# Kernel tuning notes

Hardware: AMD Instinct MI355X
Metric: run time of the kernel (lower is better)

The kernel has to match this reference:

```python
import jax, jax.numpy as jnp
import numpy as np


def setup_inputs() -> dict:
    key = jax.random.key(0)
    ks = jax.random.split(key, 6)
    B, Q, K = 4, 512, 1024
    Dq, Dk, Dv, H = 512, 512, 512, 128
    return {
        "queries": jax.random.normal(ks[0], (B, Q, Dq), dtype=jnp.float32),
        "keys": jax.random.normal(ks[1], (B, K, Dk), dtype=jnp.float32),
        "values": jax.random.normal(ks[2], (B, K, Dv), dtype=jnp.float32),
        "W_q": jax.random.normal(ks[3], (Dq, H), dtype=jnp.float32) / np.sqrt(Dq),
        "W_k": jax.random.normal(ks[4], (Dk, H), dtype=jnp.float32) / np.sqrt(Dk),
        "w_v": jax.random.normal(ks[5], (H,), dtype=jnp.float32) / np.sqrt(H),
    }


def reference(queries, keys, values, W_q, W_k, w_v):
    # Additive (Bahdanau) attention.
    q = jnp.einsum("bqd,dh->bqh", queries, W_q)          # [B,Q,H]
    k = jnp.einsum("bkd,dh->bkh", keys, W_k)             # [B,K,H]
    features = jnp.tanh(q[:, :, None, :] + k[:, None, :, :])  # [B,Q,K,H]
    scores = jnp.einsum("bqkh,h->bqk", features, w_v)    # [B,Q,K]
    attn = jax.nn.softmax(scores, axis=-1)               # [B,Q,K]
    return jnp.einsum("bqk,bkv->bqv", attn, values)      # [B,Q,Dv]
```

## Files before the change

kernel.cpp:

```cpp
#include <hip/hip_runtime.h>

#define BB   4
#define QS   512
#define KSZ  1024
#define DD   512
#define HH   128
#define DVV  512

typedef unsigned int uint;
typedef unsigned short ushort;
typedef __attribute__((ext_vector_type(8)))  short short8;
typedef __attribute__((ext_vector_type(16))) float f32x16;

__device__ __forceinline__ float rcp_fast(float x)  { return __builtin_amdgcn_rcpf(x); }
__device__ __forceinline__ float exp2_fast(float x) { return __builtin_amdgcn_exp2f(x); }

__device__ __forceinline__ void split1(float v, ushort& h, ushort& l) {
    uint u = __float_as_uint(v);
    h = (ushort)(u >> 16);
    float r = v - __uint_as_float(u & 0xffff0000u);
    l = (ushort)(__float_as_uint(r) >> 16);
}

#define NSQ  (BB * QS * DD / 4 / 256)
#define NSK  (BB * KSZ * DD / 4 / 256)
#define NWT  128
#define NPJ  192
#define NVT  (BB * (KSZ / 32) * (DVV / 32))

__global__ __launch_bounds__(256) void split_kernel(
    const float* __restrict__ q, const float* __restrict__ k,
    const float* __restrict__ Wq, const float* __restrict__ Wk,
    ushort* __restrict__ qh, ushort* __restrict__ ql,
    ushort* __restrict__ kh, ushort* __restrict__ kl,
    ushort* __restrict__ wqh, ushort* __restrict__ wql,
    ushort* __restrict__ wkh, ushort* __restrict__ wkl)
{
    const int id  = blockIdx.x;
    const int tid = threadIdx.x;

    if (id < NSQ + NSK) {
        const float* src; ushort* dh; ushort* dl; size_t i;
        if (id < NSQ) { src = q; dh = qh; dl = ql; i = (size_t)id * 256 + tid; }
        else          { src = k; dh = kh; dl = kl; i = (size_t)(id - NSQ) * 256 + tid; }
        float4 v = ((const float4*)src)[i];
        ushort h0,h1,h2,h3,l0,l1,l2,l3;
        split1(v.x,h0,l0); split1(v.y,h1,l1); split1(v.z,h2,l2); split1(v.w,h3,l3);
        *(ushort4*)&dh[i * 4] = make_ushort4(h0,h1,h2,h3);
        *(ushort4*)&dl[i * 4] = make_ushort4(l0,l1,l2,l3);
        return;
    }
    __shared__ float Ts[32][33];
    int t = id - (NSQ + NSK);
    const float* W; ushort* dh; ushort* dl;
    if (t < 64) { W = Wq; dh = wqh; dl = wql; }
    else        { W = Wk; dh = wkh; dl = wkl; t -= 64; }
    const int d0 = (t >> 2) * 32, h0 = (t & 3) * 32;
    {
        const int dd = tid >> 3, c4 = (tid & 7) * 4;
        float4 v = *(const float4*)&W[(size_t)(d0 + dd) * HH + h0 + c4];
        Ts[dd][c4 + 0] = v.x; Ts[dd][c4 + 1] = v.y;
        Ts[dd][c4 + 2] = v.z; Ts[dd][c4 + 3] = v.w;
    }
    __syncthreads();
    {
        const int hh = tid >> 3, d4 = (tid & 7) * 4;
        ushort h[4], l[4];
        #pragma unroll
        for (int i = 0; i < 4; i++) split1(Ts[d4 + i][hh], h[i], l[i]);
        size_t o = (size_t)(h0 + hh) * DD + d0 + d4;
        *(ushort4*)&dh[o] = make_ushort4(h[0], h[1], h[2], h[3]);
        *(ushort4*)&dl[o] = make_ushort4(l[0], l[1], l[2], l[3]);
    }
}

__global__ __launch_bounds__(256) void projvt_kernel(
    const ushort* __restrict__ qh, const ushort* __restrict__ ql,
    const ushort* __restrict__ kh, const ushort* __restrict__ kl,
    const ushort* __restrict__ wqh, const ushort* __restrict__ wql,
    const ushort* __restrict__ wkh, const ushort* __restrict__ wkl,
    const float* __restrict__ val,
    float* __restrict__ eq, float* __restrict__ ek,
    ushort* __restrict__ vhi, ushort* __restrict__ vlo)
{
    const int id  = blockIdx.x;
    const int tid = threadIdx.x;

    if (id >= NPJ) {
        __shared__ float Ts[32][33];
        const int t   = id - NPJ;
        const int b   = t >> 9;
        const int rem = t & 511;
        const int k0  = (rem >> 4) * 32;
        const int n0  = (rem & 15) * 32;
        {
            const int kk = tid >> 3, n4 = (tid & 7) * 4;
            float4 v = *(const float4*)&val[((size_t)b * KSZ + k0 + kk) * DVV + n0 + n4];
            Ts[kk][n4 + 0] = v.x; Ts[kk][n4 + 1] = v.y;
            Ts[kk][n4 + 2] = v.z; Ts[kk][n4 + 3] = v.w;
        }
        __syncthreads();
        {
            const int nn = tid >> 3, k4 = (tid & 7) * 4;
            ushort h[4], l[4];
            #pragma unroll
            for (int i = 0; i < 4; i++) split1(Ts[k4 + i][nn], h[i], l[i]);
            size_t o = ((size_t)b * DVV + n0 + nn) * KSZ + k0 + k4;
            *(ushort4*)&vhi[o] = make_ushort4(h[0], h[1], h[2], h[3]);
            *(ushort4*)&vlo[o] = make_ushort4(l[0], l[1], l[2], l[3]);
        }
        return;
    }

    const int w = tid >> 6, lane = tid & 63;
    const int row = lane & 31, kg = lane >> 5;
    const int gw = id * 4 + w;

    const ushort *pa_h, *pa_l, *pb_h, *pb_l; float* op; int m0, nt;
    if (gw < 256) {
        m0 = (gw >> 2) * 32; nt = gw & 3;
        pa_h = qh; pa_l = ql; pb_h = wqh; pb_l = wql; op = eq;
    } else {
        const int g = gw - 256;
        m0 = (g >> 2) * 32; nt = g & 3;
        pa_h = kh; pa_l = kl; pb_h = wkh; pb_l = wkl; op = ek;
    }

    const ushort* ah_p = pa_h + (size_t)(m0 + row) * DD + kg * 8;
    const ushort* al_p = pa_l + (size_t)(m0 + row) * DD + kg * 8;
    const ushort* bh_p = pb_h + (size_t)(nt * 32 + row) * DD + kg * 8;
    const ushort* bl_p = pb_l + (size_t)(nt * 32 + row) * DD + kg * 8;

    f32x16 acc;
    #pragma unroll
    for (int i = 0; i < 16; i++) acc[i] = 0.f;

    #pragma unroll 8
    for (int ks = 0; ks < DD; ks += 16) {
        short8 ah = *(const short8*)(ah_p + ks);
        short8 al = *(const short8*)(al_p + ks);
        short8 bh = *(const short8*)(bh_p + ks);
        short8 bl = *(const short8*)(bl_p + ks);
        acc = __builtin_amdgcn_mfma_f32_32x32x16_bf16(ah, bh, acc, 0, 0, 0);
        acc = __builtin_amdgcn_mfma_f32_32x32x16_bf16(ah, bl, acc, 0, 0, 0);
        acc = __builtin_amdgcn_mfma_f32_32x32x16_bf16(al, bh, acc, 0, 0, 0);
    }

    const float C2L = 2.8853900817779268f;
    float* ob = op + (size_t)m0 * HH + nt * 32;
    #pragma unroll
    for (int r = 0; r < 16; r++) {
        const int rb = (r & 3) + 8 * (r >> 2) + 4 * kg;
        ob[(size_t)rb * HH + row] = exp2_fast(acc[r] * C2L);
    }
}

__global__ __launch_bounds__(256) void scores_kernel(
    const float* __restrict__ eq, const float* __restrict__ ek,
    const float* __restrict__ wv, ushort* __restrict__ Phi,
    ushort* __restrict__ Plo, float* __restrict__ rsp)
{
    __shared__ float eqs[64][68];
    __shared__ float eks[64][68];

    const int tid = threadIdx.x;
    const int b  = blockIdx.z;
    const int q0 = blockIdx.y * 64;
    const int k0 = blockIdx.x * 64;

    const float* eqb = eq + ((size_t)b * QS  + q0) * HH;
    const float* ekb = ek + ((size_t)b * KSZ + k0) * HH;

    const int tk = tid & 15;
    const int tq = tid >> 4;

    float acc[4][4] = {};

    for (int hc = 0; hc < HH; hc += 64) {
        __syncthreads();
        #pragma unroll
        for (int i = 0; i < 4; i++) {
            int f = tid + i * 256;
            int row = f >> 4, c4 = f & 15;
            *(float4*)&eqs[row][c4 * 4] =
                *(const float4*)&eqb[(size_t)row * HH + hc + c4 * 4];
            *(float4*)&eks[row][c4 * 4] =
                *(const float4*)&ekb[(size_t)row * HH + hc + c4 * 4];
        }
        __syncthreads();

        for (int h0 = 0; h0 < 64; h0 += 4) {
            float4 wv4 = *(const float4*)&wv[hc + h0];
            float4 eq4[4], ek4[4];
            #pragma unroll
            for (int j = 0; j < 4; j++) {
                eq4[j] = *(const float4*)&eqs[tq + 16 * j][h0];
                ek4[j] = *(const float4*)&eks[tk + 16 * j][h0];
            }
            #pragma unroll
            for (int jq = 0; jq < 4; jq++) {
                #pragma unroll
                for (int jk = 0; jk < 4; jk++) {
                    float u0 = fminf(fmaf(eq4[jq].x, ek4[jk].x, 1.0f), 3e7f);
                    float u1 = fminf(fmaf(eq4[jq].y, ek4[jk].y, 1.0f), 3e7f);
                    float u2 = fminf(fmaf(eq4[jq].z, ek4[jk].z, 1.0f), 3e7f);
                    float u3 = fminf(fmaf(eq4[jq].w, ek4[jk].w, 1.0f), 3e7f);
                    float p01 = u0 * u1, p23 = u2 * u3;
                    float n01 = fmaf(wv4.x, u1, wv4.y * u0);
                    float n23 = fmaf(wv4.z, u3, wv4.w * u2);
                    float N = fmaf(n01, p23, n23 * p01);
                    acc[jq][jk] = fmaf(N, rcp_fast(p01 * p23), acc[jq][jk]);
                }
            }
        }
    }

    const float CN = -2.8853900817779268f;
    ushort* ph = Phi + ((size_t)b * QS + q0) * KSZ + k0;
    ushort* pl = Plo + ((size_t)b * QS + q0) * KSZ + k0;
    #pragma unroll
    for (int jq = 0; jq < 4; jq++) {
        float rowp = 0.f;
        #pragma unroll
        for (int jk = 0; jk < 4; jk++) {
            float pv_ = exp2_fast(acc[jq][jk] * CN);
            ushort hh, ll; split1(pv_, hh, ll);
            size_t o = (size_t)(tq + 16 * jq) * KSZ + tk + 16 * jk;
            ph[o] = hh; pl[o] = ll;
            rowp += pv_;
        }
        #pragma unroll
        for (int m = 8; m; m >>= 1) rowp += __shfl_xor(rowp, m);
        if ((tid & 15) == 0)
            rsp[((size_t)b * QS + q0 + tq + 16 * jq) * 16 + blockIdx.x] = rowp;
    }
}

__global__ __launch_bounds__(256) void pv_mfma_kernel(
    const ushort* __restrict__ Phi, const ushort* __restrict__ Plo,
    const ushort* __restrict__ vhi, const ushort* __restrict__ vlo,
    const float* __restrict__ rsp, float* __restrict__ outp)
{
    __shared__ float invs[32];
    __shared__ float accs[2][32][33];

    const int id  = blockIdx.x;
    const int x   = id & 7;
    const int j   = id >> 3;
    const int bm  = x * 8 + (j >> 3);
    const int ntp = j & 7;
    const int b   = bm >> 4, mt = bm & 15;

    const int tid = threadIdx.x, w = tid >> 6, lane = tid & 63;
    const int row = lane & 31, kg = lane >> 5;

    if (tid < 32) {
        const float* rp = rsp + ((size_t)b * QS + mt * 32 + tid) * 16;
        float s = 0.f;
        #pragma unroll
        for (int i = 0; i < 16; i++) s += rp[i];
        invs[tid] = rcp_fast(s);
    }

    const int nt  = ntp * 2 + (w >> 1);
    const int kh0 = (w & 1) * (KSZ / 2);

    const ushort* pah = Phi + ((size_t)b * QS  + mt * 32 + row) * KSZ + kh0 + kg * 8;
    const ushort* pal = Plo + ((size_t)b * QS  + mt * 32 + row) * KSZ + kh0 + kg * 8;
    const ushort* bhp = vhi + ((size_t)b * DVV + nt * 32 + row) * KSZ + kh0 + kg * 8;
    const ushort* blp = vlo + ((size_t)b * DVV + nt * 32 + row) * KSZ + kh0 + kg * 8;

    f32x16 acc0, acc1;
    #pragma unroll
    for (int i = 0; i < 16; i++) { acc0[i] = 0.f; acc1[i] = 0.f; }

    #pragma unroll 4
    for (int kb = 0; kb < KSZ / 2; kb += 32) {
        short8 a0h = *(const short8*)(pah + kb);
        short8 a0l = *(const short8*)(pal + kb);
        short8 v0h = *(const short8*)(bhp + kb);
        short8 v0l = *(const short8*)(blp + kb);
        short8 a1h = *(const short8*)(pah + kb + 16);
        short8 a1l = *(const short8*)(pal + kb + 16);
        short8 v1h = *(const short8*)(bhp + kb + 16);
        short8 v1l = *(const short8*)(blp + kb + 16);
        acc0 = __builtin_amdgcn_mfma_f32_32x32x16_bf16(a0h, v0h, acc0, 0, 0, 0);
        acc1 = __builtin_amdgcn_mfma_f32_32x32x16_bf16(a1h, v1h, acc1, 0, 0, 0);
        acc0 = __builtin_amdgcn_mfma_f32_32x32x16_bf16(a0h, v0l, acc0, 0, 0, 0);
        acc1 = __builtin_amdgcn_mfma_f32_32x32x16_bf16(a1h, v1l, acc1, 0, 0, 0);
        acc0 = __builtin_amdgcn_mfma_f32_32x32x16_bf16(a0l, v0h, acc0, 0, 0, 0);
        acc1 = __builtin_amdgcn_mfma_f32_32x32x16_bf16(a1l, v1h, acc1, 0, 0, 0);
    }
    #pragma unroll
    for (int i = 0; i < 16; i++) acc0[i] += acc1[i];

    if (w & 1) {
        #pragma unroll
        for (int r = 0; r < 16; r++)
            accs[w >> 1][(r & 3) + 8 * (r >> 2) + 4 * kg][row] = acc0[r];
    }
    __syncthreads();
    if (!(w & 1)) {
        float* ob = outp + ((size_t)b * QS + mt * 32) * DVV + nt * 32;
        #pragma unroll
        for (int r = 0; r < 16; r++) {
            const int rb = (r & 3) + 8 * (r >> 2) + 4 * kg;
            float v = acc0[r] + accs[w >> 1][rb][row];
            ob[(size_t)rb * DVV + row] = v * invs[rb];
        }
    }
}

extern "C" void kernel_launch(void* const* d_in, const int* in_sizes, int n_in,
                              void* d_out, int out_size, void* d_ws, size_t ws_size,
                              hipStream_t stream)
{
    const float* queries = (const float*)d_in[0];
    const float* keys    = (const float*)d_in[1];
    const float* values  = (const float*)d_in[2];
    const float* Wq      = (const float*)d_in[3];
    const float* Wk      = (const float*)d_in[4];
    const float* wv      = (const float*)d_in[5];
    float* out = (float*)d_out;

    float*  eq  = (float*)d_ws;
    float*  ek  = eq + (size_t)BB * QS * HH;
    float*  rsp = ek + (size_t)BB * KSZ * HH;
    ushort* Phi = (ushort*)(rsp + (size_t)BB * QS * 16);
    ushort* Plo = Phi + (size_t)BB * QS * KSZ;
    ushort* vhi = Plo + (size_t)BB * QS * KSZ;
    ushort* vlo = vhi + (size_t)BB * KSZ * DVV;
    ushort* qh  = vlo + (size_t)BB * KSZ * DVV;
    ushort* ql  = qh  + (size_t)BB * QS * DD;
    ushort* kh  = ql  + (size_t)BB * QS * DD;
    ushort* kl  = kh  + (size_t)BB * KSZ * DD;
    ushort* wqh = kl  + (size_t)BB * KSZ * DD;
    ushort* wql = wqh + (size_t)HH * DD;
    ushort* wkh = wql + (size_t)HH * DD;
    ushort* wkl = wkh + (size_t)HH * DD;

    split_kernel<<<dim3(NSQ + NSK + NWT), 256, 0, stream>>>(
        queries, keys, Wq, Wk, qh, ql, kh, kl, wqh, wql, wkh, wkl);

    projvt_kernel<<<dim3(NPJ + NVT), 256, 0, stream>>>(
        qh, ql, kh, kl, wqh, wql, wkh, wkl, values, eq, ek, vhi, vlo);

    scores_kernel<<<dim3(KSZ / 64, QS / 64, BB), 256, 0, stream>>>(
        eq, ek, wv, Phi, Plo, rsp);

    pv_mfma_kernel<<<dim3(512), 256, 0, stream>>>(Phi, Plo, vhi, vlo, rsp, out);
}
```

Measured before the change: 161.2 us.

## Widen scores tile along K and stage PV operands through LDS with prefetch

The scores kernel now computes a 64x128 tile per block, with 8 key columns per thread instead of 4, halving the grid and the number of row-sum partials. The PV kernel is restructured from a per-wave split-K design that read operands directly from global memory to a 64x64 output tile per block. Hi/lo P and V chunks are staged in shared memory, with the next chunk prefetched into registers while MFMAs run. This aims to raise operand reuse and cut redundant global traffic, at the cost of more registers, two barriers per chunk and only 256 blocks.

```diff
diff --git a/kernel.cpp b/kernel.cpp
--- a/kernel.cpp
+++ b/kernel.cpp
@@ -9,6 +9,7 @@
 
 typedef unsigned int uint;
 typedef unsigned short ushort;
+typedef unsigned long long ull;
 typedef __attribute__((ext_vector_type(8)))  short short8;
 typedef __attribute__((ext_vector_type(16))) float f32x16;
 
@@ -161,12 +162,12 @@
     ushort* __restrict__ Plo, float* __restrict__ rsp)
 {
     __shared__ float eqs[64][68];
-    __shared__ float eks[64][68];
+    __shared__ float eks[128][68];
 
     const int tid = threadIdx.x;
     const int b  = blockIdx.z;
     const int q0 = blockIdx.y * 64;
-    const int k0 = blockIdx.x * 64;
+    const int k0 = blockIdx.x * 128;
 
     const float* eqb = eq + ((size_t)b * QS  + q0) * HH;
     const float* ekb = ek + ((size_t)b * KSZ + k0) * HH;
@@ -174,7 +175,7 @@
     const int tk = tid & 15;
     const int tq = tid >> 4;
 
-    float acc[4][4] = {};
+    float acc[4][8] = {};
 
     for (int hc = 0; hc < HH; hc += 64) {
         __syncthreads();
@@ -184,6 +185,11 @@
             int row = f >> 4, c4 = f & 15;
             *(float4*)&eqs[row][c4 * 4] =
                 *(const float4*)&eqb[(size_t)row * HH + hc + c4 * 4];
+        }
+        #pragma unroll
+        for (int i = 0; i < 8; i++) {
+            int f = tid + i * 256;
+            int row = f >> 4, c4 = f & 15;
             *(float4*)&eks[row][c4 * 4] =
                 *(const float4*)&ekb[(size_t)row * HH + hc + c4 * 4];
         }
@@ -191,20 +197,19 @@
 
         for (int h0 = 0; h0 < 64; h0 += 4) {
             float4 wv4 = *(const float4*)&wv[hc + h0];
-            float4 eq4[4], ek4[4];
+            float4 eq4[4], ek8[8];
             #pragma unroll
-            for (int j = 0; j < 4; j++) {
-                eq4[j] = *(const float4*)&eqs[tq + 16 * j][h0];
-                ek4[j] = *(const float4*)&eks[tk + 16 * j][h0];
-            }
+            for (int j = 0; j < 4; j++) eq4[j] = *(const float4*)&eqs[tq + 16 * j][h0];
+            #pragma unroll
+            for (int j = 0; j < 8; j++) ek8[j] = *(const float4*)&eks[tk + 16 * j][h0];
             #pragma unroll
             for (int jq = 0; jq < 4; jq++) {
                 #pragma unroll
-                for (int jk = 0; jk < 4; jk++) {
-                    float u0 = fminf(fmaf(eq4[jq].x, ek4[jk].x, 1.0f), 3e7f);
-                    float u1 = fminf(fmaf(eq4[jq].y, ek4[jk].y, 1.0f), 3e7f);
-                    float u2 = fminf(fmaf(eq4[jq].z, ek4[jk].z, 1.0f), 3e7f);
-                    float u3 = fminf(fmaf(eq4[jq].w, ek4[jk].w, 1.0f), 3e7f);
+                for (int jk = 0; jk < 8; jk++) {
+                    float u0 = fminf(fmaf(eq4[jq].x, ek8[jk].x, 1.0f), 3e7f);
+                    float u1 = fminf(fmaf(eq4[jq].y, ek8[jk].y, 1.0f), 3e7f);
+                    float u2 = fminf(fmaf(eq4[jq].z, ek8[jk].z, 1.0f), 3e7f);
+                    float u3 = fminf(fmaf(eq4[jq].w, ek8[jk].w, 1.0f), 3e7f);
                     float p01 = u0 * u1, p23 = u2 * u3;
                     float n01 = fmaf(wv4.x, u1, wv4.y * u0);
                     float n23 = fmaf(wv4.z, u3, wv4.w * u2);
@@ -222,7 +227,7 @@
     for (int jq = 0; jq < 4; jq++) {
         float rowp = 0.f;
         #pragma unroll
-        for (int jk = 0; jk < 4; jk++) {
+        for (int jk = 0; jk < 8; jk++) {
             float pv_ = exp2_fast(acc[jq][jk] * CN);
             ushort hh, ll; split1(pv_, hh, ll);
             size_t o = (size_t)(tq + 16 * jq) * KSZ + tk + 16 * jk;
@@ -232,7 +237,7 @@
         #pragma unroll
         for (int m = 8; m; m >>= 1) rowp += __shfl_xor(rowp, m);
         if ((tid & 15) == 0)
-            rsp[((size_t)b * QS + q0 + tq + 16 * jq) * 16 + blockIdx.x] = rowp;
+            rsp[((size_t)b * QS + q0 + tq + 16 * jq) * 8 + blockIdx.x] = rowp;
     }
 }
 
@@ -241,74 +246,94 @@
     const ushort* __restrict__ vhi, const ushort* __restrict__ vlo,
     const float* __restrict__ rsp, float* __restrict__ outp)
 {
-    __shared__ float invs[32];
-    __shared__ float accs[2][32][33];
+    __shared__ ushort PhS[64][68];
+    __shared__ ushort PlS[64][68];
+    __shared__ ushort VhS[64][68];
+    __shared__ ushort VlS[64][68];
+    __shared__ float invs[64];
 
     const int id  = blockIdx.x;
     const int x   = id & 7;
-    const int j   = id >> 3;
-    const int bm  = x * 8 + (j >> 3);
-    const int ntp = j & 7;
-    const int b   = bm >> 4, mt = bm & 15;
+    const int g   = id >> 3;
+    const int bmg = x * 4 + (g >> 3);
+    const int b   = bmg >> 3, mt = bmg & 7;
+    const int ntB = g & 7;
 
     const int tid = threadIdx.x, w = tid >> 6, lane = tid & 63;
-    const int row = lane & 31, kg = lane >> 5;
-
-    if (tid < 32) {
-        const float* rp = rsp + ((size_t)b * QS + mt * 32 + tid) * 16;
+    const int col = lane & 31, kg = lane >> 5;
+
+    if (tid < 64) {
+        const float* rp = rsp + ((size_t)b * QS + mt * 64 + tid) * 8;
         float s = 0.f;
         #pragma unroll
-        for (int i = 0; i < 16; i++) s += rp[i];
+        for (int i = 0; i < 8; i++) s += rp[i];
         invs[tid] = rcp_fast(s);
     }
 
-    const int nt  = ntp * 2 + (w >> 1);
-    const int kh0 = (w & 1) * (KSZ / 2);
-
-    const ushort* pah = Phi + ((size_t)b * QS  + mt * 32 + row) * KSZ + kh0 + kg * 8;
-    const ushort* pal = Plo + ((size_t)b * QS  + mt * 32 + row) * KSZ + kh0 + kg * 8;
-    const ushort* bhp = vhi + ((size_t)b * DVV + nt * 32 + row) * KSZ + kh0 + kg * 8;
-    const ushort* blp = vlo + ((size_t)b * DVV + nt * 32 + row) * KSZ + kh0 + kg * 8;
-
-    f32x16 acc0, acc1;
-    #pragma unroll
-    for (int i = 0; i < 16; i++) { acc0[i] = 0.f; acc1[i] = 0.f; }
-
-    #pragma unroll 4
-    for (int kb = 0; kb < KSZ / 2; kb += 32) {
-        short8 a0h = *(const short8*)(pah + kb);
-        short8 a0l = *(const short8*)(pal + kb);
-        short8 v0h = *(const short8*)(bhp + kb);
-        short8 v0l = *(const short8*)(blp + kb);
-        short8 a1h = *(const short8*)(pah + kb + 16);
-        short8 a1l = *(const short8*)(pal + kb + 16);
-        short8 v1h = *(const short8*)(bhp + kb + 16);
-        short8 v1l = *(const short8*)(blp + kb + 16);
-        acc0 = __builtin_amdgcn_mfma_f32_32x32x16_bf16(a0h, v0h, acc0, 0, 0, 0);
-        acc1 = __builtin_amdgcn_mfma_f32_32x32x16_bf16(a1h, v1h, acc1, 0, 0, 0);
-        acc0 = __builtin_amdgcn_mfma_f32_32x32x16_bf16(a0h, v0l, acc0, 0, 0, 0);
-        acc1 = __builtin_amdgcn_mfma_f32_32x32x16_bf16(a1h, v1l, acc1, 0, 0, 0);
-        acc0 = __builtin_amdgcn_mfma_f32_32x32x16_bf16(a0l, v0h, acc0, 0, 0, 0);
-        acc1 = __builtin_amdgcn_mfma_f32_32x32x16_bf16(a1l, v1h, acc1, 0, 0, 0);
-    }
-    #pragma unroll
-    for (int i = 0; i < 16; i++) acc0[i] += acc1[i];
-
-    if (w & 1) {
-        #pragma unroll
-        for (int r = 0; r < 16; r++)
-            accs[w >> 1][(r & 3) + 8 * (r >> 2) + 4 * kg][row] = acc0[r];
-    }
+    const int wm = (w & 1) * 32, wn = (w >> 1) * 32;
+
+    const int sr = tid >> 2, cc = (tid & 3) * 16;
+    const ushort* gPh = Phi + ((size_t)b * QS  + mt * 64 + sr) * KSZ + cc;
+    const ushort* gPl = Plo + ((size_t)b * QS  + mt * 64 + sr) * KSZ + cc;
+    const ushort* gVh = vhi + ((size_t)b * DVV + ntB * 64 + sr) * KSZ + cc;
+    const ushort* gVl = vlo + ((size_t)b * DVV + ntB * 64 + sr) * KSZ + cc;
+
+    f32x16 acc;
+    #pragma unroll
+    for (int i = 0; i < 16; i++) acc[i] = 0.f;
+
+    uint4 rph0, rph1, rpl0, rpl1, rvh0, rvh1, rvl0, rvl1;
+#define LOADC(kc) \
+    rph0 = *(const uint4*)(gPh + (kc)); rph1 = *(const uint4*)(gPh + (kc) + 8); \
+    rpl0 = *(const uint4*)(gPl + (kc)); rpl1 = *(const uint4*)(gPl + (kc) + 8); \
+    rvh0 = *(const uint4*)(gVh + (kc)); rvh1 = *(const uint4*)(gVh + (kc) + 8); \
+    rvl0 = *(const uint4*)(gVl + (kc)); rvl1 = *(const uint4*)(gVl + (kc) + 8);
+#define STOREC() { \
+    ull* dPh = (ull*)&PhS[sr][cc]; ull* dPl = (ull*)&PlS[sr][cc]; \
+    ull* dVh = (ull*)&VhS[sr][cc]; ull* dVl = (ull*)&VlS[sr][cc]; \
+    dPh[0] = ((ull*)&rph0)[0]; dPh[1] = ((ull*)&rph0)[1]; \
+    dPh[2] = ((ull*)&rph1)[0]; dPh[3] = ((ull*)&rph1)[1]; \
+    dPl[0] = ((ull*)&rpl0)[0]; dPl[1] = ((ull*)&rpl0)[1]; \
+    dPl[2] = ((ull*)&rpl1)[0]; dPl[3] = ((ull*)&rpl1)[1]; \
+    dVh[0] = ((ull*)&rvh0)[0]; dVh[1] = ((ull*)&rvh0)[1]; \
+    dVh[2] = ((ull*)&rvh1)[0]; dVh[3] = ((ull*)&rvh1)[1]; \
+    dVl[0] = ((ull*)&rvl0)[0]; dVl[1] = ((ull*)&rvl0)[1]; \
+    dVl[2] = ((ull*)&rvl1)[0]; dVl[3] = ((ull*)&rvl1)[1]; }
+
+    LOADC(0);
+    STOREC();
     __syncthreads();
-    if (!(w & 1)) {
-        float* ob = outp + ((size_t)b * QS + mt * 32) * DVV + nt * 32;
-        #pragma unroll
-        for (int r = 0; r < 16; r++) {
-            const int rb = (r & 3) + 8 * (r >> 2) + 4 * kg;
-            float v = acc0[r] + accs[w >> 1][rb][row];
-            ob[(size_t)rb * DVV + row] = v * invs[rb];
-        }
-    }
+
+    for (int c = 0; c < 16; c++) {
+        if (c < 15) { LOADC((c + 1) * 64); }
+        #pragma unroll
+        for (int kk = 0; kk < 4; kk++) {
+            const int off = kk * 16 + kg * 8;
+            short8 ah, al, vh, vl;
+            { const ull* p = (const ull*)&PhS[wm + col][off];
+              ((ull*)&ah)[0] = p[0]; ((ull*)&ah)[1] = p[1]; }
+            { const ull* p = (const ull*)&PlS[wm + col][off];
+              ((ull*)&al)[0] = p[0]; ((ull*)&al)[1] = p[1]; }
+            { const ull* p = (const ull*)&VhS[wn + col][off];
+              ((ull*)&vh)[0] = p[0]; ((ull*)&vh)[1] = p[1]; }
+            { const ull* p = (const ull*)&VlS[wn + col][off];
+              ((ull*)&vl)[0] = p[0]; ((ull*)&vl)[1] = p[1]; }
+            acc = __builtin_amdgcn_mfma_f32_32x32x16_bf16(ah, vh, acc, 0, 0, 0);
+            acc = __builtin_amdgcn_mfma_f32_32x32x16_bf16(ah, vl, acc, 0, 0, 0);
+            acc = __builtin_amdgcn_mfma_f32_32x32x16_bf16(al, vh, acc, 0, 0, 0);
+        }
+        __syncthreads();
+        if (c < 15) { STOREC(); __syncthreads(); }
+    }
+
+    float* ob = outp + ((size_t)b * QS + mt * 64 + wm) * DVV + ntB * 64 + wn;
+    #pragma unroll
+    for (int r = 0; r < 16; r++) {
+        const int rb = (r & 3) + 8 * (r >> 2) + 4 * kg;
+        ob[(size_t)rb * DVV + col] = acc[r] * invs[wm + rb];
+    }
+#undef LOADC
+#undef STOREC
 }
 
 extern "C" void kernel_launch(void* const* d_in, const int* in_sizes, int n_in,
@@ -326,7 +351,7 @@
     float*  eq  = (float*)d_ws;
     float*  ek  = eq + (size_t)BB * QS * HH;
     float*  rsp = ek + (size_t)BB * KSZ * HH;
-    ushort* Phi = (ushort*)(rsp + (size_t)BB * QS * 16);
+    ushort* Phi = (ushort*)(rsp + (size_t)BB * QS * 8);
     ushort* Plo = Phi + (size_t)BB * QS * KSZ;
     ushort* vhi = Plo + (size_t)BB * QS * KSZ;
     ushort* vlo = vhi + (size_t)BB * KSZ * DVV;
@@ -345,8 +370,8 @@
     projvt_kernel<<<dim3(NPJ + NVT), 256, 0, stream>>>(
         qh, ql, kh, kl, wqh, wql, wkh, wkl, values, eq, ek, vhi, vlo);
 
-    scores_kernel<<<dim3(KSZ / 64, QS / 64, BB), 256, 0, stream>>>(
+    scores_kernel<<<dim3(KSZ / 128, QS / 64, BB), 256, 0, stream>>>(
         eq, ek, wv, Phi, Plo, rsp);
 
-    pv_mfma_kernel<<<dim3(512), 256, 0, stream>>>(Phi, Plo, vhi, vlo, rsp, out);
-}
+    pv_mfma_kernel<<<dim3(256), 256, 0, stream>>>(Phi, Plo, vhi, vlo, rsp, out);
+}
```

Result: faster. 154.3 us (-4.3%).
